# Kernel tuning notes

Hardware: AMD Instinct MI355X
Metric: run time of the kernel (lower is better)

The kernel has to match this reference:

```python
import jax, jax.numpy as jnp
import numpy as np

T, B, F, H, P = 256, 512, 256, 512, 12  # seq len, batch, feature_dim, hidden_dim, p_interval


def setup_inputs() -> dict:
    key = jax.random.key(0)
    ks = jax.random.split(key, 9)
    s = 1.0 / np.sqrt(F + H)  # torch Linear default init scale
    def lin(k):
        kw, kb = jax.random.split(k)
        W = jax.random.uniform(kw, (F + H, H), jnp.float32, -s, s)
        b = jax.random.uniform(kb, (H,), jnp.float32, -s, s)
        return W, b
    Wf, bf = lin(ks[0])
    Wi, bi = lin(ks[1])
    Wo, bo = lin(ks[2])
    Wg, bg = lin(ks[3])
    x = jax.random.normal(ks[4], (T, B, F), jnp.float32)
    return {"x": x, "Wf": Wf, "bf": bf, "Wi": Wi, "bi": bi,
            "Wo": Wo, "bo": bo, "Wg": Wg, "bg": bg}


def _slstm(x, Wf, bf, Wi, bi, Wo, bo, Wg, bg):
    Tn, Bn, _ = x.shape
    h0 = jnp.zeros((P, Bn, H), x.dtype)
    # NOTE: original torch code reassigns c to a 2D [B,H] tensor after step 0,
    # so c[t % P] indexes a batch ROW (shape [H]) that broadcasts. At t=0 the
    # slice is all-zeros either way, so carrying a 2D c is exactly faithful.
    c0 = jnp.zeros((Bn, H), x.dtype)

    def step(carry, inp):
        h, c = carry
        x_t, t = inp
        idx = t % P
        xc = jnp.concatenate([x_t, h[idx]], axis=1)  # [B, F+H]
        f = jax.nn.softmax(xc @ Wf + bf, axis=1)
        i = jax.nn.softmax(xc @ Wi + bi, axis=1)
        o = jax.nn.softmax(xc @ Wo + bo, axis=1)
        g = jnp.tanh(xc @ Wg + bg)
        c_new = jnp.tanh(f * c[idx] + i * g)  # c[idx]: row [H], broadcasts over B
        h = h.at[idx].set(o * c_new)
        return (h, c_new), None

    (h, _), _ = jax.lax.scan(step, (h0, c0), (x, jnp.arange(Tn)))
    return h[(Tn - 1) % P]


def reference(x, Wf, bf, Wi, bi, Wo, bo, Wg, bg):
    return _slstm(x, Wf, bf, Wi, bi, Wo, bo, Wg, bg)
```

## Files before the change

### kernel.cpp

```cpp
#include <hip/hip_runtime.h>

typedef unsigned short u16;
typedef unsigned int   u32;

typedef __attribute__((ext_vector_type(8))) short bf16x8;
typedef __attribute__((ext_vector_type(16))) float f32x16;

__device__ __forceinline__ u16 f2bf(float v) {
    u32 u = __float_as_uint(v);
    u32 r = (u + 0x7fffu + ((u >> 16) & 1u)) >> 16;
    return (u16)r;
}
__device__ __forceinline__ float bf2f(u16 h) { return __uint_as_float(((u32)h) << 16); }

__device__ __forceinline__ float ftanh(float x) {
    float e = __expf(2.0f * x);
    return 1.0f - 2.0f * __builtin_amdgcn_rcpf(e + 1.0f);
}

__device__ __forceinline__ void gl2lds16(const void* g, void* l) {
    __builtin_amdgcn_global_load_lds(
        (const __attribute__((address_space(1))) void*)g,
        (__attribute__((address_space(3))) void*)l, 16, 0, 0);
}

__global__ void init_k(u16* __restrict__ hh, u16* __restrict__ hl, float* __restrict__ cb) {
    int i = blockIdx.x * 256 + threadIdx.x;
    hh[i] = 0; hl[i] = 0;
    if (i < 2 * 512) cb[i] = 0.0f;
}

__global__ void pack_w(const float* __restrict__ Wf, const float* __restrict__ bf_,
                       const float* __restrict__ Wi, const float* __restrict__ bi_,
                       const float* __restrict__ Wo, const float* __restrict__ bo_,
                       const float* __restrict__ Wg, const float* __restrict__ bg_,
                       u16* __restrict__ wth, u16* __restrict__ wtl, float* __restrict__ bias4) {
    int idx = blockIdx.x * 256 + threadIdx.x;
    int n = idx / 768, k = idx - n * 768;
    int gate = n >> 9, col = n & 511;
    const float* W = (gate == 0) ? Wf : (gate == 1) ? Wi : (gate == 2) ? Wo : Wg;
    float v = W[k * 512 + col];
    u16 h = f2bf(v);
    wth[idx] = h;
    wtl[idx] = f2bf(v - bf2f(h));
    if (k == 0) {
        const float* bb = (gate == 0) ? bf_ : (gate == 1) ? bi_ : (gate == 2) ? bo_ : bg_;
        bias4[n] = bb[col];
    }
}

__global__ void split_x(const float* __restrict__ src, u16* __restrict__ oh, u16* __restrict__ ol) {
    int i = blockIdx.x * 256 + threadIdx.x;
    float4 v = ((const float4*)src)[i];
    u16 hx = f2bf(v.x), hy = f2bf(v.y), hz = f2bf(v.z), hw = f2bf(v.w);
    u16 lx = f2bf(v.x - bf2f(hx)), ly = f2bf(v.y - bf2f(hy));
    u16 lz = f2bf(v.z - bf2f(hz)), lw = f2bf(v.w - bf2f(hw));
    uint2 hv; hv.x = (u32)hx | ((u32)hy << 16); hv.y = (u32)hz | ((u32)hw << 16);
    uint2 lv; lv.x = (u32)lx | ((u32)ly << 16); lv.y = (u32)lz | ((u32)lw << 16);
    ((uint2*)oh)[i] = hv;
    ((uint2*)ol)[i] = lv;
}

#define BK 32
__global__ __launch_bounds__(256, 3) void gemm_x3(
    const u16* __restrict__ xh, const u16* __restrict__ xl,
    const u16* __restrict__ hh, const u16* __restrict__ hl,
    const u16* __restrict__ wth, const u16* __restrict__ wtl,
    const float* __restrict__ bias4, float* __restrict__ lg) {
    __shared__ __align__(16) u16 Ah[128 * BK];
    __shared__ __align__(16) u16 Al[128 * BK];
    __shared__ __align__(16) u16 Bh[128 * BK];
    __shared__ __align__(16) u16 Bl[128 * BK];

    const int tid = threadIdx.x;
    const int wid = tid >> 6, lane = tid & 63;
    const int bm = blockIdx.x, bn = blockIdx.y;
    const int s = bm >> 2;
    const int b0 = (bm & 3) * 128;
    const int laneR = lane >> 2;
    const int laneC = (lane & 3) * 8;

    u16* lds = (wid == 0) ? Ah : (wid == 1) ? Al : (wid == 2) ? Bh : Bl;
    const u16* xp = (wid == 0) ? xh : xl;
    const u16* hp = (wid == 0) ? hh : hl;
    const u16* wp = (wid == 2) ? wth : wtl;
    const u16* xrow = xp + (size_t)(s * 512 + b0) * 256 + laneR * 256 + laneC;
    const u16* hrow = hp + (size_t)(s * 512 + b0) * 512 + laneR * 512 + laneC;
    const u16* wrow = wp + (size_t)(bn * 128) * 768 + laneR * 768 + laneC;

    const int wm = wid >> 1, wn = wid & 1;
    const int l32 = lane & 31, khalf = lane >> 5;

    f32x16 acc[2][2];
#pragma unroll
    for (int i = 0; i < 2; i++)
#pragma unroll
        for (int j = 0; j < 2; j++)
#pragma unroll
            for (int r = 0; r < 16; ++r) acc[i][j][r] = 0.f;

    for (int k0 = 0; k0 < 768; k0 += BK) {
        __syncthreads();
        if (wid < 2) {
            if (k0 < 256) {
                const u16* src = xrow + k0;
#pragma unroll
                for (int r = 0; r < 8; ++r) gl2lds16(src + r * 16 * 256, lds + r * 16 * BK);
            } else {
                const u16* src = hrow + (k0 - 256);
#pragma unroll
                for (int r = 0; r < 8; ++r) gl2lds16(src + r * 16 * 512, lds + r * 16 * BK);
            }
        } else {
            const u16* src = wrow + k0;
#pragma unroll
            for (int r = 0; r < 8; ++r) gl2lds16(src + r * 16 * 768, lds + r * 16 * BK);
        }
        __syncthreads();

        bf16x8 a_h[2][2], a_l[2][2], b_h[2][2], b_l[2][2];
#pragma unroll
        for (int t = 0; t < 2; ++t)
#pragma unroll
            for (int ks = 0; ks < 2; ++ks) {
                int ko = ks * 16 + khalf * 8;
                a_h[t][ks] = *(const bf16x8*)&Ah[(wm * 64 + t * 32 + l32) * BK + ko];
                a_l[t][ks] = *(const bf16x8*)&Al[(wm * 64 + t * 32 + l32) * BK + ko];
                b_h[t][ks] = *(const bf16x8*)&Bh[(wn * 64 + t * 32 + l32) * BK + ko];
                b_l[t][ks] = *(const bf16x8*)&Bl[(wn * 64 + t * 32 + l32) * BK + ko];
            }
#pragma unroll
        for (int ks = 0; ks < 2; ++ks)
#pragma unroll
            for (int i = 0; i < 2; ++i)
#pragma unroll
                for (int j = 0; j < 2; ++j) {
                    acc[i][j] = __builtin_amdgcn_mfma_f32_32x32x16_bf16(a_h[i][ks], b_h[j][ks], acc[i][j], 0, 0, 0);
                    acc[i][j] = __builtin_amdgcn_mfma_f32_32x32x16_bf16(a_h[i][ks], b_l[j][ks], acc[i][j], 0, 0, 0);
                    acc[i][j] = __builtin_amdgcn_mfma_f32_32x32x16_bf16(a_l[i][ks], b_h[j][ks], acc[i][j], 0, 0, 0);
                }
    }

#pragma unroll
    for (int j = 0; j < 2; ++j) {
        int n = bn * 128 + wn * 64 + j * 32 + l32;
        float bv = bias4[n];
#pragma unroll
        for (int i = 0; i < 2; ++i) {
            int rbase = wm * 64 + i * 32 + 4 * khalf;
#pragma unroll
            for (int r = 0; r < 16; ++r) {
                int row = rbase + (r & 3) + 8 * (r >> 2);
                __builtin_nontemporal_store(acc[i][j][r] + bv,
                    &lg[(size_t)(bm * 128 + row) * 2048 + n]);
            }
        }
    }
}

__device__ __forceinline__ void chain_step(const float* __restrict__ lg, int j, int lane, float r[8]) {
    int rowb = (j + 1) % 12;
    const float* base = lg + (size_t)(j * 512 + rowb) * 2048 + lane * 8;
    float f[8], iv[8], g[8];
#pragma unroll
    for (int u = 0; u < 8; ++u) { f[u] = base[u]; iv[u] = base[512 + u]; g[u] = base[1536 + u]; }
    float mf = -1e30f, mi = -1e30f;
#pragma unroll
    for (int u = 0; u < 8; ++u) { mf = fmaxf(mf, f[u]); mi = fmaxf(mi, iv[u]); }
#pragma unroll
    for (int o = 32; o; o >>= 1) { mf = fmaxf(mf, __shfl_xor(mf, o)); mi = fmaxf(mi, __shfl_xor(mi, o)); }
    float sf = 0.f, si = 0.f;
#pragma unroll
    for (int u = 0; u < 8; ++u) {
        f[u] = __expf(f[u] - mf); sf += f[u];
        iv[u] = __expf(iv[u] - mi); si += iv[u];
    }
#pragma unroll
    for (int o = 32; o; o >>= 1) { sf += __shfl_xor(sf, o); si += __shfl_xor(si, o); }
    float rf = __builtin_amdgcn_rcpf(sf), ri = __builtin_amdgcn_rcpf(si);
#pragma unroll
    for (int u = 0; u < 8; ++u) {
        float gg = ftanh(g[u]);
        r[u] = ftanh(f[u] * rf * r[u] + iv[u] * ri * gg);
    }
}

__global__ __launch_bounds__(256) void gates_k(
    const float* __restrict__ lg, float* __restrict__ cb,
    u16* __restrict__ hh, u16* __restrict__ hl,
    float* __restrict__ out, int t0, int S, int rd, int wr) {
    __shared__ float rsh[512];
    const int widx = threadIdx.x >> 6, lane = threadIdx.x & 63;
    const int s = (S - 1) - (blockIdx.x >> 7);
    const int b = (blockIdx.x & 127) * 4 + widx;
    const int t = t0 + s;

    if (widx == 0) {
        float r[8];
#pragma unroll
        for (int u = 0; u < 8; ++u) r[u] = cb[rd * 512 + lane * 8 + u];
        for (int j = 0; j < s; ++j) chain_step(lg, j, lane, r);
#pragma unroll
        for (int u = 0; u < 8; ++u) rsh[lane * 8 + u] = r[u];
        if ((int)blockIdx.x == 127 && t0 + S < 256) {
            chain_step(lg, S - 1, lane, r);
#pragma unroll
            for (int u = 0; u < 8; ++u) cb[wr * 512 + lane * 8 + u] = r[u];
        }
    }
    __syncthreads();

    const float* row = lg + (size_t)(s * 512 + b) * 2048 + lane * 8;
    float f[8], iv[8], ov[8], g[8];
#pragma unroll
    for (int u = 0; u < 8; ++u) {
        f[u] = row[u]; iv[u] = row[512 + u]; ov[u] = row[1024 + u]; g[u] = row[1536 + u];
    }
    float mf = -1e30f, mi = -1e30f, mo = -1e30f;
#pragma unroll
    for (int u = 0; u < 8; ++u) { mf = fmaxf(mf, f[u]); mi = fmaxf(mi, iv[u]); mo = fmaxf(mo, ov[u]); }
#pragma unroll
    for (int o = 32; o; o >>= 1) {
        mf = fmaxf(mf, __shfl_xor(mf, o));
        mi = fmaxf(mi, __shfl_xor(mi, o));
        mo = fmaxf(mo, __shfl_xor(mo, o));
    }
    float sf = 0.f, si = 0.f, so = 0.f;
#pragma unroll
    for (int u = 0; u < 8; ++u) {
        f[u] = __expf(f[u] - mf); sf += f[u];
        iv[u] = __expf(iv[u] - mi); si += iv[u];
        ov[u] = __expf(ov[u] - mo); so += ov[u];
    }
#pragma unroll
    for (int o = 32; o; o >>= 1) {
        sf += __shfl_xor(sf, o); si += __shfl_xor(si, o); so += __shfl_xor(so, o);
    }
    float rf = __builtin_amdgcn_rcpf(sf), ri = __builtin_amdgcn_rcpf(si), ro = __builtin_amdgcn_rcpf(so);
    float hout[8];
#pragma unroll
    for (int u = 0; u < 8; ++u) {
        float rr = rsh[lane * 8 + u];
        float gg = ftanh(g[u]);
        float cv = ftanh(f[u] * rf * rr + iv[u] * ri * gg);
        hout[u] = ov[u] * ro * cv;
    }
    u32 hhp[4], hlp[4];
#pragma unroll
    for (int u = 0; u < 4; ++u) {
        u16 h0 = f2bf(hout[2 * u]), h1 = f2bf(hout[2 * u + 1]);
        u16 l0 = f2bf(hout[2 * u] - bf2f(h0)), l1 = f2bf(hout[2 * u + 1] - bf2f(h1));
        hhp[u] = (u32)h0 | ((u32)h1 << 16);
        hlp[u] = (u32)l0 | ((u32)l1 << 16);
    }
    size_t hb = ((size_t)(s * 512 + b)) * 512 + lane * 8;
    *(uint4*)&hh[hb] = make_uint4(hhp[0], hhp[1], hhp[2], hhp[3]);
    *(uint4*)&hl[hb] = make_uint4(hlp[0], hlp[1], hlp[2], hlp[3]);
    if (t == 255) {
        float* op = out + (size_t)b * 512 + lane * 8;
#pragma unroll
        for (int u = 0; u < 8; ++u) op[u] = hout[u];
    }
}

extern "C" void kernel_launch(void* const* d_in, const int* in_sizes, int n_in,
                              void* d_out, int out_size, void* d_ws, size_t ws_size,
                              hipStream_t stream) {
    const float* x   = (const float*)d_in[0];
    const float* Wf  = (const float*)d_in[1];
    const float* bf_ = (const float*)d_in[2];
    const float* Wi  = (const float*)d_in[3];
    const float* bi_ = (const float*)d_in[4];
    const float* Wo  = (const float*)d_in[5];
    const float* bo_ = (const float*)d_in[6];
    const float* Wg  = (const float*)d_in[7];
    const float* bg_ = (const float*)d_in[8];
    float* out = (float*)d_out;

    char* p = (char*)d_ws;
    u16* xh  = (u16*)p; p += 134217728;
    u16* xl  = (u16*)p; p += 134217728;
    u16* wth = (u16*)p; p += 3145728;
    u16* wtl = (u16*)p; p += 3145728;
    u16* hh  = (u16*)p; p += 6291456;
    u16* hl  = (u16*)p; p += 6291456;
    float* bias4 = (float*)p; p += 8192;
    float* cb    = (float*)p; p += 4096;
    float* lg    = (float*)p; p += 50331648;

    init_k<<<12288, 256, 0, stream>>>(hh, hl, cb);
    pack_w<<<6144, 256, 0, stream>>>(Wf, bf_, Wi, bi_, Wo, bo_, Wg, bg_, wth, wtl, bias4);
    split_x<<<32768, 256, 0, stream>>>(x, xh, xl);

    for (int blk = 0; blk < 22; ++blk) {
        int t0 = blk * 12;
        int S = (256 - t0 >= 12) ? 12 : (256 - t0);
        gemm_x3<<<dim3(S * 4, 16), 256, 0, stream>>>(
            xh + (size_t)t0 * 512 * 256, xl + (size_t)t0 * 512 * 256,
            hh, hl, wth, wtl, bias4, lg);
        gates_k<<<S * 128, 256, 0, stream>>>(lg, cb, hh, hl, out, t0, S, blk & 1, (blk + 1) & 1);
    }
}
```

Baseline: 2.029 ms.

## Rewrite split-bf16 GEMM with double-buffered LDS, larger tiles and grid swizzle

Replaces the 128x128 single-buffered GEMM with a 512-thread kernel using 192x256 tiles and double-buffered LDS. Global-to-LDS loads for the next k-tile are issued in two halves interleaved with the MFMA phases, using explicit vmcnt waits and barriers plus raised priority around the MFMA blocks. A 1D grid remapped across 8 column groups aims to improve L2 reuse. The M dimension is now bounds-checked because 192 does not divide evenly into it. The intent is to hide memory latency and raise MFMA utilisation, at the cost of more LDS and register pressure and more fragile hand-written synchronisation.

```diff
diff --git a/kernel.cpp b/kernel.cpp
--- a/kernel.cpp
+++ b/kernel.cpp
@@ -61,98 +61,170 @@
     ((uint2*)ol)[i] = lv;
 }
 
-#define BK 32
-__global__ __launch_bounds__(256, 3) void gemm_x3(
+#define KTILES 24
+#define BUFHALF 28672
+
+__global__ __launch_bounds__(512, 2) void gemm_p(
     const u16* __restrict__ xh, const u16* __restrict__ xl,
     const u16* __restrict__ hh, const u16* __restrict__ hl,
     const u16* __restrict__ wth, const u16* __restrict__ wtl,
-    const float* __restrict__ bias4, float* __restrict__ lg) {
-    __shared__ __align__(16) u16 Ah[128 * BK];
-    __shared__ __align__(16) u16 Al[128 * BK];
-    __shared__ __align__(16) u16 Bh[128 * BK];
-    __shared__ __align__(16) u16 Bl[128 * BK];
+    const float* __restrict__ bias4, float* __restrict__ lg,
+    int Mvalid, int gx) {
+    __shared__ __align__(16) u16 smem[2 * BUFHALF];
 
     const int tid = threadIdx.x;
     const int wid = tid >> 6, lane = tid & 63;
-    const int bm = blockIdx.x, bn = blockIdx.y;
-    const int s = bm >> 2;
-    const int b0 = (bm & 3) * 128;
-    const int laneR = lane >> 2;
-    const int laneC = (lane & 3) * 8;
-
-    u16* lds = (wid == 0) ? Ah : (wid == 1) ? Al : (wid == 2) ? Bh : Bl;
-    const u16* xp = (wid == 0) ? xh : xl;
-    const u16* hp = (wid == 0) ? hh : hl;
-    const u16* wp = (wid == 2) ? wth : wtl;
-    const u16* xrow = xp + (size_t)(s * 512 + b0) * 256 + laneR * 256 + laneC;
-    const u16* hrow = hp + (size_t)(s * 512 + b0) * 512 + laneR * 512 + laneC;
-    const u16* wrow = wp + (size_t)(bn * 128) * 768 + laneR * 768 + laneC;
-
-    const int wm = wid >> 1, wn = wid & 1;
     const int l32 = lane & 31, khalf = lane >> 5;
-
-    f32x16 acc[2][2];
-#pragma unroll
-    for (int i = 0; i < 2; i++)
-#pragma unroll
-        for (int j = 0; j < 2; j++)
+    const int wm = wid >> 2, wn = wid & 3;
+
+    const int wg = (blockIdx.x & 7) * gx + (blockIdx.x >> 3);
+    const int bm = wg % gx, bn = wg / gx;
+
+    const int laneK = (lane >> 4) * 8;
+    const int lr = lane & 15;
+    const u16* sp0[7]; const u16* sp1[7]; u32 slds[7]; bool sA[7];
+#pragma unroll
+    for (int j = 0; j < 7; ++j) {
+        int slot = wid * 7 + j;
+        int o, c;
+        if (slot < 12)      { o = 0; c = slot; }
+        else if (slot < 24) { o = 1; c = slot - 12; }
+        else if (slot < 40) { o = 2; c = slot - 24; }
+        else                { o = 3; c = slot - 40; }
+        if (o < 2) {
+            int row = bm * 192 + c * 16 + lr;
+            if (row >= Mvalid) row = Mvalid - 1;
+            sp0[j] = ((o == 0) ? xh : xl) + (size_t)row * 256 + laneK;
+            sp1[j] = ((o == 0) ? hh : hl) + (size_t)row * 512 + laneK;
+            sA[j] = true;
+            slds[j] = (o ? 6144u : 0u) + (u32)c * 512u;
+        } else {
+            int row = bn * 256 + c * 16 + lr;
+            sp0[j] = ((o == 2) ? wth : wtl) + (size_t)row * 768 + laneK;
+            sp1[j] = sp0[j];
+            sA[j] = false;
+            slds[j] = ((o == 2) ? 12288u : 20480u) + (u32)c * 512u;
+        }
+    }
+
+    u32 offA[3], offB[2];
+#pragma unroll
+    for (int i = 0; i < 3; ++i) {
+        int r = wm * 96 + i * 32 + l32;
+        offA[i] = (u32)((r >> 4) * 512 + (r & 15) * 8);
+    }
+#pragma unroll
+    for (int j = 0; j < 2; ++j) {
+        int r = wn * 64 + j * 32 + l32;
+        offB[j] = (u32)((r >> 4) * 512 + (r & 15) * 8);
+    }
+
+    f32x16 acc[3][2];
+#pragma unroll
+    for (int i = 0; i < 3; ++i)
+#pragma unroll
+        for (int j = 0; j < 2; ++j)
 #pragma unroll
             for (int r = 0; r < 16; ++r) acc[i][j][r] = 0.f;
 
-    for (int k0 = 0; k0 < 768; k0 += BK) {
-        __syncthreads();
-        if (wid < 2) {
-            if (k0 < 256) {
-                const u16* src = xrow + k0;
-#pragma unroll
-                for (int r = 0; r < 8; ++r) gl2lds16(src + r * 16 * 256, lds + r * 16 * BK);
-            } else {
-                const u16* src = hrow + (k0 - 256);
-#pragma unroll
-                for (int r = 0; r < 8; ++r) gl2lds16(src + r * 16 * 512, lds + r * 16 * BK);
-            }
+#pragma unroll
+    for (int j = 0; j < 7; ++j) gl2lds16(sp0[j], smem + slds[j]);
+
+#pragma unroll 2
+    for (int kk = 0; kk < KTILES; ++kk) {
+        u16* bufc = smem + (kk & 1) * BUFHALF;
+        u16* bufo = smem + ((kk & 1) ^ 1) * BUFHALF;
+        const int kn = (kk + 1) * 32;
+
+        if (kk < KTILES - 1) {
+#pragma unroll
+            for (int j = 0; j < 4; ++j) {
+                const u16* src = sA[j] ? ((kn < 256) ? sp0[j] + kn : sp1[j] + (kn - 256))
+                                       : (sp0[j] + kn);
+                gl2lds16(src, bufo + slds[j]);
+            }
+            asm volatile("s_waitcnt vmcnt(4)" ::: "memory");
         } else {
-            const u16* src = wrow + k0;
-#pragma unroll
-            for (int r = 0; r < 8; ++r) gl2lds16(src + r * 16 * 768, lds + r * 16 * BK);
-        }
-        __syncthreads();
-
-        bf16x8 a_h[2][2], a_l[2][2], b_h[2][2], b_l[2][2];
-#pragma unroll
-        for (int t = 0; t < 2; ++t)
-#pragma unroll
-            for (int ks = 0; ks < 2; ++ks) {
-                int ko = ks * 16 + khalf * 8;
-                a_h[t][ks] = *(const bf16x8*)&Ah[(wm * 64 + t * 32 + l32) * BK + ko];
-                a_l[t][ks] = *(const bf16x8*)&Al[(wm * 64 + t * 32 + l32) * BK + ko];
-                b_h[t][ks] = *(const bf16x8*)&Bh[(wn * 64 + t * 32 + l32) * BK + ko];
-                b_l[t][ks] = *(const bf16x8*)&Bl[(wn * 64 + t * 32 + l32) * BK + ko];
-            }
-#pragma unroll
-        for (int ks = 0; ks < 2; ++ks)
-#pragma unroll
-            for (int i = 0; i < 2; ++i)
-#pragma unroll
-                for (int j = 0; j < 2; ++j) {
-                    acc[i][j] = __builtin_amdgcn_mfma_f32_32x32x16_bf16(a_h[i][ks], b_h[j][ks], acc[i][j], 0, 0, 0);
-                    acc[i][j] = __builtin_amdgcn_mfma_f32_32x32x16_bf16(a_h[i][ks], b_l[j][ks], acc[i][j], 0, 0, 0);
-                    acc[i][j] = __builtin_amdgcn_mfma_f32_32x32x16_bf16(a_l[i][ks], b_h[j][ks], acc[i][j], 0, 0, 0);
-                }
+            asm volatile("s_waitcnt vmcnt(0)" ::: "memory");
+        }
+        asm volatile("s_barrier" ::: "memory");
+
+        bf16x8 ah[3], al[3], bh[2], bl[2];
+        {
+            const u32 q = (u32)(khalf) * 128u;
+#pragma unroll
+            for (int i = 0; i < 3; ++i) {
+                ah[i] = *(const bf16x8*)(bufc + offA[i] + q);
+                al[i] = *(const bf16x8*)(bufc + 6144 + offA[i] + q);
+            }
+#pragma unroll
+            for (int j = 0; j < 2; ++j) {
+                bh[j] = *(const bf16x8*)(bufc + 12288 + offB[j] + q);
+                bl[j] = *(const bf16x8*)(bufc + 20480 + offB[j] + q);
+            }
+        }
+        asm volatile("s_waitcnt lgkmcnt(0)" ::: "memory");
+        __builtin_amdgcn_s_setprio(1);
+#pragma unroll
+        for (int i = 0; i < 3; ++i)
+#pragma unroll
+            for (int j = 0; j < 2; ++j) {
+                acc[i][j] = __builtin_amdgcn_mfma_f32_32x32x16_bf16(ah[i], bh[j], acc[i][j], 0, 0, 0);
+                acc[i][j] = __builtin_amdgcn_mfma_f32_32x32x16_bf16(ah[i], bl[j], acc[i][j], 0, 0, 0);
+                acc[i][j] = __builtin_amdgcn_mfma_f32_32x32x16_bf16(al[i], bh[j], acc[i][j], 0, 0, 0);
+            }
+        __builtin_amdgcn_s_setprio(0);
+        asm volatile("s_barrier" ::: "memory");
+
+        if (kk < KTILES - 1) {
+#pragma unroll
+            for (int j = 4; j < 7; ++j) {
+                const u16* src = sA[j] ? ((kn < 256) ? sp0[j] + kn : sp1[j] + (kn - 256))
+                                       : (sp0[j] + kn);
+                gl2lds16(src, bufo + slds[j]);
+            }
+        }
+        {
+            const u32 q = (u32)(2 + khalf) * 128u;
+#pragma unroll
+            for (int i = 0; i < 3; ++i) {
+                ah[i] = *(const bf16x8*)(bufc + offA[i] + q);
+                al[i] = *(const bf16x8*)(bufc + 6144 + offA[i] + q);
+            }
+#pragma unroll
+            for (int j = 0; j < 2; ++j) {
+                bh[j] = *(const bf16x8*)(bufc + 12288 + offB[j] + q);
+                bl[j] = *(const bf16x8*)(bufc + 20480 + offB[j] + q);
+            }
+        }
+        asm volatile("s_barrier" ::: "memory");
+        asm volatile("s_waitcnt lgkmcnt(0)" ::: "memory");
+        __builtin_amdgcn_s_setprio(1);
+#pragma unroll
+        for (int i = 0; i < 3; ++i)
+#pragma unroll
+            for (int j = 0; j < 2; ++j) {
+                acc[i][j] = __builtin_amdgcn_mfma_f32_32x32x16_bf16(ah[i], bh[j], acc[i][j], 0, 0, 0);
+                acc[i][j] = __builtin_amdgcn_mfma_f32_32x32x16_bf16(ah[i], bl[j], acc[i][j], 0, 0, 0);
+                acc[i][j] = __builtin_amdgcn_mfma_f32_32x32x16_bf16(al[i], bh[j], acc[i][j], 0, 0, 0);
+            }
+        __builtin_amdgcn_s_setprio(0);
+        asm volatile("s_barrier" ::: "memory");
     }
 
 #pragma unroll
     for (int j = 0; j < 2; ++j) {
-        int n = bn * 128 + wn * 64 + j * 32 + l32;
+        int n = bn * 256 + wn * 64 + j * 32 + l32;
         float bv = bias4[n];
 #pragma unroll
-        for (int i = 0; i < 2; ++i) {
-            int rbase = wm * 64 + i * 32 + 4 * khalf;
+        for (int i = 0; i < 3; ++i) {
+            int rbase = bm * 192 + wm * 96 + i * 32 + 4 * khalf;
 #pragma unroll
             for (int r = 0; r < 16; ++r) {
                 int row = rbase + (r & 3) + 8 * (r >> 2);
-                __builtin_nontemporal_store(acc[i][j][r] + bv,
-                    &lg[(size_t)(bm * 128 + row) * 2048 + n]);
+                if (row < Mvalid)
+                    __builtin_nontemporal_store(acc[i][j][r] + bv,
+                        &lg[(size_t)row * 2048 + n]);
             }
         }
     }
@@ -295,9 +367,11 @@
     for (int blk = 0; blk < 22; ++blk) {
         int t0 = blk * 12;
         int S = (256 - t0 >= 12) ? 12 : (256 - t0);
-        gemm_x3<<<dim3(S * 4, 16), 256, 0, stream>>>(
+        int M = S * 512;
+        int gx = (M + 191) / 192;
+        gemm_p<<<gx * 8, 512, 0, stream>>>(
             xh + (size_t)t0 * 512 * 256, xl + (size_t)t0 * 512 * 256,
-            hh, hl, wth, wtl, bias4, lg);
+            hh, hl, wth, wtl, bias4, lg, M, gx);
         gates_k<<<S * 128, 256, 0, stream>>>(lg, cb, hh, hl, out, t0, S, blk & 1, (blk + 1) & 1);
     }
 }
```

Result: slower. 2.104 ms (+3.7%).

## Rewrite split-bf16 GEMM with larger tiles, triple-buffered swizzled LDS, and pre-concatenated K

Applied to the files above, without the earlier changes.

Replaces the 128x128 tile GEMM with a 192x256 tile using 8 waves and 512 threads. The three-product split-bf16 scheme is reformulated as one long K=2304 GEMM: the weights are packed with hi/lo/hi copies so the A side can stream xh/xl/hh/hl segments. A and B tiles are loaded into LDS asynchronously with an XOR swizzle, A is triple-buffered and B double-buffered, and loads are overlapped with MFMA using waitcnt and setprio. Blocks are remapped onto XCDs and edge rows are masked. The cost is three times the weight storage and more complex, hand-scheduled synchronization.

```diff
diff --git a/kernel.cpp b/kernel.cpp
--- a/kernel.cpp
+++ b/kernel.cpp
@@ -30,19 +30,25 @@
     if (i < 2 * 512) cb[i] = 0.0f;
 }
 
-__global__ void pack_w(const float* __restrict__ Wf, const float* __restrict__ bf_,
-                       const float* __restrict__ Wi, const float* __restrict__ bi_,
-                       const float* __restrict__ Wo, const float* __restrict__ bo_,
-                       const float* __restrict__ Wg, const float* __restrict__ bg_,
-                       u16* __restrict__ wth, u16* __restrict__ wtl, float* __restrict__ bias4) {
+__global__ void pack_wq(const float* __restrict__ Wf, const float* __restrict__ bf_,
+                        const float* __restrict__ Wi, const float* __restrict__ bi_,
+                        const float* __restrict__ Wo, const float* __restrict__ bo_,
+                        const float* __restrict__ Wg, const float* __restrict__ bg_,
+                        u16* __restrict__ wq, float* __restrict__ bias4) {
     int idx = blockIdx.x * 256 + threadIdx.x;
     int n = idx / 768, k = idx - n * 768;
     int gate = n >> 9, col = n & 511;
     const float* W = (gate == 0) ? Wf : (gate == 1) ? Wi : (gate == 2) ? Wo : Wg;
     float v = W[k * 512 + col];
     u16 h = f2bf(v);
-    wth[idx] = h;
-    wtl[idx] = f2bf(v - bf2f(h));
+    u16 l = f2bf(v - bf2f(h));
+    size_t base = (size_t)n * 2304;
+    if (k < 256) {
+        wq[base + k] = h; wq[base + 512 + k] = h; wq[base + 256 + k] = l;
+    } else {
+        int d = k - 256;
+        wq[base + 768 + d] = h; wq[base + 1792 + d] = h; wq[base + 1280 + d] = l;
+    }
     if (k == 0) {
         const float* bb = (gate == 0) ? bf_ : (gate == 1) ? bi_ : (gate == 2) ? bo_ : bg_;
         bias4[n] = bb[col];
@@ -61,98 +67,161 @@
     ((uint2*)ol)[i] = lv;
 }
 
-#define BK 32
-__global__ __launch_bounds__(256, 3) void gemm_x3(
+#define KT 36
+__global__ __launch_bounds__(512, 2) void gemm_q(
     const u16* __restrict__ xh, const u16* __restrict__ xl,
     const u16* __restrict__ hh, const u16* __restrict__ hl,
-    const u16* __restrict__ wth, const u16* __restrict__ wtl,
-    const float* __restrict__ bias4, float* __restrict__ lg) {
-    __shared__ __align__(16) u16 Ah[128 * BK];
-    __shared__ __align__(16) u16 Al[128 * BK];
-    __shared__ __align__(16) u16 Bh[128 * BK];
-    __shared__ __align__(16) u16 Bl[128 * BK];
+    const u16* __restrict__ wq, const float* __restrict__ bias4,
+    float* __restrict__ lg, int Mvalid, int gx) {
+    __shared__ __align__(16) u16 smem[69632];
 
     const int tid = threadIdx.x;
     const int wid = tid >> 6, lane = tid & 63;
-    const int bm = blockIdx.x, bn = blockIdx.y;
-    const int s = bm >> 2;
-    const int b0 = (bm & 3) * 128;
-    const int laneR = lane >> 2;
-    const int laneC = (lane & 3) * 8;
-
-    u16* lds = (wid == 0) ? Ah : (wid == 1) ? Al : (wid == 2) ? Bh : Bl;
-    const u16* xp = (wid == 0) ? xh : xl;
-    const u16* hp = (wid == 0) ? hh : hl;
-    const u16* wp = (wid == 2) ? wth : wtl;
-    const u16* xrow = xp + (size_t)(s * 512 + b0) * 256 + laneR * 256 + laneC;
-    const u16* hrow = hp + (size_t)(s * 512 + b0) * 512 + laneR * 512 + laneC;
-    const u16* wrow = wp + (size_t)(bn * 128) * 768 + laneR * 768 + laneC;
-
-    const int wm = wid >> 1, wn = wid & 1;
     const int l32 = lane & 31, khalf = lane >> 5;
-
-    f32x16 acc[2][2];
-#pragma unroll
-    for (int i = 0; i < 2; i++)
-#pragma unroll
-        for (int j = 0; j < 2; j++)
+    const int wm = wid >> 2, wn = wid & 3;
+
+    int bm, bn;
+    if (gx == 32) { int xcd = blockIdx.x & 7, r = blockIdx.x >> 3; bm = xcd * 4 + (r & 3); bn = r >> 2; }
+    else          { bm = blockIdx.x % gx; bn = blockIdx.x / gx; }
+
+    const int lr8 = lane >> 3;
+    const int ksw = ((lane & 7) ^ (lr8 & 7)) * 8;
+
+    int arowc[3]; size_t brow[4];
+#pragma unroll
+    for (int c = 0; c < 3; ++c) {
+        int row = bm * 192 + (wid * 3 + c) * 8 + lr8;
+        if (row >= Mvalid) row = Mvalid - 1;
+        arowc[c] = row;
+    }
+#pragma unroll
+    for (int c = 0; c < 4; ++c)
+        brow[c] = (size_t)(bn * 256 + (wid * 4 + c) * 8 + lr8) * 2304;
+
+#define STAGE_A(kt, dstoff) do {                                              \
+        int kt_ = (kt); const u16* base_; int str_, ko_;                      \
+        if (kt_ < 12) { base_ = (kt_ >= 8) ? xl : xh; str_ = 256; ko_ = (kt_ & 3) * 64; } \
+        else { int sub_ = kt_ - 12; base_ = (sub_ >= 16) ? hl : hh; str_ = 512; ko_ = (sub_ & 7) * 64; } \
+        _Pragma("unroll")                                                     \
+        for (int c_ = 0; c_ < 3; ++c_)                                        \
+            gl2lds16(base_ + (size_t)arowc[c_] * str_ + ko_ + ksw,            \
+                     smem + (dstoff) + (wid * 3 + c_) * 512 + lane * 8);      \
+    } while (0)
+
+#define STAGE_B(kt, dstoff) do {                                              \
+        _Pragma("unroll")                                                     \
+        for (int c_ = 0; c_ < 4; ++c_)                                        \
+            gl2lds16(wq + brow[c_] + (kt) * 64 + ksw,                         \
+                     smem + (dstoff) + (wid * 4 + c_) * 512 + lane * 8);      \
+    } while (0)
+
+    u32 offA[3][4], offB[2][4];
+#pragma unroll
+    for (int i = 0; i < 3; ++i) {
+        int row = wm * 96 + i * 32 + l32;
+        u32 rsw = (u32)(row & 7) << 3;
+#pragma unroll
+        for (int ks = 0; ks < 4; ++ks)
+            offA[i][ks] = (u32)row * 64 + (((u32)(ks * 16 + khalf * 8)) ^ rsw);
+    }
+#pragma unroll
+    for (int j = 0; j < 2; ++j) {
+        int row = wn * 64 + j * 32 + l32;
+        u32 rsw = (u32)(row & 7) << 3;
+#pragma unroll
+        for (int ks = 0; ks < 4; ++ks)
+            offB[j][ks] = (u32)row * 64 + (((u32)(ks * 16 + khalf * 8)) ^ rsw);
+    }
+
+    f32x16 acc[3][2];
+#pragma unroll
+    for (int i = 0; i < 3; ++i)
+#pragma unroll
+        for (int j = 0; j < 2; ++j)
 #pragma unroll
             for (int r = 0; r < 16; ++r) acc[i][j][r] = 0.f;
 
-    for (int k0 = 0; k0 < 768; k0 += BK) {
-        __syncthreads();
-        if (wid < 2) {
-            if (k0 < 256) {
-                const u16* src = xrow + k0;
-#pragma unroll
-                for (int r = 0; r < 8; ++r) gl2lds16(src + r * 16 * 256, lds + r * 16 * BK);
-            } else {
-                const u16* src = hrow + (k0 - 256);
-#pragma unroll
-                for (int r = 0; r < 8; ++r) gl2lds16(src + r * 16 * 512, lds + r * 16 * BK);
-            }
+    STAGE_A(0, 0);
+    STAGE_B(0, 36864);
+    STAGE_A(1, 12288);
+
+    int aoff = 0;
+    for (int kt = 0; kt < KT; ++kt) {
+        const int boff = 36864 + ((kt & 1) << 14);
+        if (kt + 1 < KT) {
+            STAGE_B(kt + 1, 36864 + (((kt + 1) & 1) << 14));
+            asm volatile("s_waitcnt vmcnt(7)" ::: "memory");
         } else {
-            const u16* src = wrow + k0;
-#pragma unroll
-            for (int r = 0; r < 8; ++r) gl2lds16(src + r * 16 * 768, lds + r * 16 * BK);
+            asm volatile("s_waitcnt vmcnt(0)" ::: "memory");
         }
-        __syncthreads();
-
-        bf16x8 a_h[2][2], a_l[2][2], b_h[2][2], b_l[2][2];
-#pragma unroll
-        for (int t = 0; t < 2; ++t)
-#pragma unroll
-            for (int ks = 0; ks < 2; ++ks) {
-                int ko = ks * 16 + khalf * 8;
-                a_h[t][ks] = *(const bf16x8*)&Ah[(wm * 64 + t * 32 + l32) * BK + ko];
-                a_l[t][ks] = *(const bf16x8*)&Al[(wm * 64 + t * 32 + l32) * BK + ko];
-                b_h[t][ks] = *(const bf16x8*)&Bh[(wn * 64 + t * 32 + l32) * BK + ko];
-                b_l[t][ks] = *(const bf16x8*)&Bl[(wn * 64 + t * 32 + l32) * BK + ko];
-            }
+        __builtin_amdgcn_s_barrier();
+        __builtin_amdgcn_sched_barrier(0);
+
+        const u16* At = smem + aoff;
+        const u16* Bt = smem + boff;
+
+        bf16x8 a0[3][2], b0[2][2];
+#pragma unroll
+        for (int i = 0; i < 3; ++i)
+#pragma unroll
+            for (int ks = 0; ks < 2; ++ks) a0[i][ks] = *(const bf16x8*)(At + offA[i][ks]);
+#pragma unroll
+        for (int j = 0; j < 2; ++j)
+#pragma unroll
+            for (int ks = 0; ks < 2; ++ks) b0[j][ks] = *(const bf16x8*)(Bt + offB[j][ks]);
+        __builtin_amdgcn_s_setprio(1);
 #pragma unroll
         for (int ks = 0; ks < 2; ++ks)
 #pragma unroll
-            for (int i = 0; i < 2; ++i)
-#pragma unroll
-                for (int j = 0; j < 2; ++j) {
-                    acc[i][j] = __builtin_amdgcn_mfma_f32_32x32x16_bf16(a_h[i][ks], b_h[j][ks], acc[i][j], 0, 0, 0);
-                    acc[i][j] = __builtin_amdgcn_mfma_f32_32x32x16_bf16(a_h[i][ks], b_l[j][ks], acc[i][j], 0, 0, 0);
-                    acc[i][j] = __builtin_amdgcn_mfma_f32_32x32x16_bf16(a_l[i][ks], b_h[j][ks], acc[i][j], 0, 0, 0);
-                }
-    }
+            for (int i = 0; i < 3; ++i)
+#pragma unroll
+                for (int j = 0; j < 2; ++j)
+                    acc[i][j] = __builtin_amdgcn_mfma_f32_32x32x16_bf16(a0[i][ks], b0[j][ks], acc[i][j], 0, 0, 0);
+        __builtin_amdgcn_s_setprio(0);
+
+        if (kt + 2 < KT) {
+            int adst = aoff + 24576; if (adst >= 36864) adst -= 36864;
+            STAGE_A(kt + 2, adst);
+        }
+
+        bf16x8 a1[3][2], b1[2][2];
+#pragma unroll
+        for (int i = 0; i < 3; ++i)
+#pragma unroll
+            for (int ks = 0; ks < 2; ++ks) a1[i][ks] = *(const bf16x8*)(At + offA[i][ks + 2]);
+#pragma unroll
+        for (int j = 0; j < 2; ++j)
+#pragma unroll
+            for (int ks = 0; ks < 2; ++ks) b1[j][ks] = *(const bf16x8*)(Bt + offB[j][ks + 2]);
+        __builtin_amdgcn_s_setprio(1);
+#pragma unroll
+        for (int ks = 0; ks < 2; ++ks)
+#pragma unroll
+            for (int i = 0; i < 3; ++i)
+#pragma unroll
+                for (int j = 0; j < 2; ++j)
+                    acc[i][j] = __builtin_amdgcn_mfma_f32_32x32x16_bf16(a1[i][ks], b1[j][ks], acc[i][j], 0, 0, 0);
+        __builtin_amdgcn_s_setprio(0);
+
+        __builtin_amdgcn_s_barrier();
+        __builtin_amdgcn_sched_barrier(0);
+        aoff += 12288; if (aoff == 36864) aoff = 0;
+    }
+#undef STAGE_A
+#undef STAGE_B
 
 #pragma unroll
     for (int j = 0; j < 2; ++j) {
-        int n = bn * 128 + wn * 64 + j * 32 + l32;
+        int n = bn * 256 + wn * 64 + j * 32 + l32;
         float bv = bias4[n];
 #pragma unroll
-        for (int i = 0; i < 2; ++i) {
-            int rbase = wm * 64 + i * 32 + 4 * khalf;
+        for (int i = 0; i < 3; ++i) {
+            int rbase = bm * 192 + wm * 96 + i * 32 + 4 * khalf;
 #pragma unroll
             for (int r = 0; r < 16; ++r) {
                 int row = rbase + (r & 3) + 8 * (r >> 2);
-                __builtin_nontemporal_store(acc[i][j][r] + bv,
-                    &lg[(size_t)(bm * 128 + row) * 2048 + n]);
+                if (row < Mvalid)
+                    lg[(size_t)row * 2048 + n] = acc[i][j][r] + bv;
             }
         }
     }
@@ -280,8 +349,7 @@
     char* p = (char*)d_ws;
     u16* xh  = (u16*)p; p += 134217728;
     u16* xl  = (u16*)p; p += 134217728;
-    u16* wth = (u16*)p; p += 3145728;
-    u16* wtl = (u16*)p; p += 3145728;
+    u16* wq  = (u16*)p; p += 9437184;
     u16* hh  = (u16*)p; p += 6291456;
     u16* hl  = (u16*)p; p += 6291456;
     float* bias4 = (float*)p; p += 8192;
@@ -289,15 +357,17 @@
     float* lg    = (float*)p; p += 50331648;
 
     init_k<<<12288, 256, 0, stream>>>(hh, hl, cb);
-    pack_w<<<6144, 256, 0, stream>>>(Wf, bf_, Wi, bi_, Wo, bo_, Wg, bg_, wth, wtl, bias4);
+    pack_wq<<<6144, 256, 0, stream>>>(Wf, bf_, Wi, bi_, Wo, bo_, Wg, bg_, wq, bias4);
     split_x<<<32768, 256, 0, stream>>>(x, xh, xl);
 
     for (int blk = 0; blk < 22; ++blk) {
         int t0 = blk * 12;
         int S = (256 - t0 >= 12) ? 12 : (256 - t0);
-        gemm_x3<<<dim3(S * 4, 16), 256, 0, stream>>>(
+        int M = S * 512;
+        int gx = (M + 191) / 192;
+        gemm_q<<<gx * 8, 512, 0, stream>>>(
             xh + (size_t)t0 * 512 * 256, xl + (size_t)t0 * 512 * 256,
-            hh, hl, wth, wtl, bias4, lg);
+            hh, hl, wq, bias4, lg, M, gx);
         gates_k<<<S * 128, 256, 0, stream>>>(lg, cb, hh, hl, out, t0, S, blk & 1, (blk + 1) & 1);
     }
 }
```

Result: no change. 2.053 ms (+1.2%).

## Rewrite split-bf16 GEMM as 256x256 double-buffered K-concatenated tile kernel

Applied to the files above, without the earlier changes.

Replaces the 128x128 three-product bf16x3 GEMM with a 256x256 tile, 512-thread kernel. The three hi/lo products are folded into one longer K dimension by pre-packing the weights as [h, l, h] segments, so each MFMA pass is a plain bf16 GEMM over K=2304. The kernel adds double-buffered LDS staging with XOR swizzle, interleaved staged loads and 16x16x32 MFMAs with barriers and priority hints, and an XCD-aware block mapping. The aim is better data reuse and latency hiding. The cost is triple-sized packed weights, higher register and LDS pressure (128KB LDS), and fewer blocks per launch for the small M dimension.

```diff
diff --git a/kernel.cpp b/kernel.cpp
--- a/kernel.cpp
+++ b/kernel.cpp
@@ -4,7 +4,7 @@
 typedef unsigned int   u32;
 
 typedef __attribute__((ext_vector_type(8))) short bf16x8;
-typedef __attribute__((ext_vector_type(16))) float f32x16;
+typedef __attribute__((ext_vector_type(4))) float f32x4;
 
 __device__ __forceinline__ u16 f2bf(float v) {
     u32 u = __float_as_uint(v);
@@ -30,19 +30,25 @@
     if (i < 2 * 512) cb[i] = 0.0f;
 }
 
-__global__ void pack_w(const float* __restrict__ Wf, const float* __restrict__ bf_,
-                       const float* __restrict__ Wi, const float* __restrict__ bi_,
-                       const float* __restrict__ Wo, const float* __restrict__ bo_,
-                       const float* __restrict__ Wg, const float* __restrict__ bg_,
-                       u16* __restrict__ wth, u16* __restrict__ wtl, float* __restrict__ bias4) {
+__global__ void pack_wq(const float* __restrict__ Wf, const float* __restrict__ bf_,
+                        const float* __restrict__ Wi, const float* __restrict__ bi_,
+                        const float* __restrict__ Wo, const float* __restrict__ bo_,
+                        const float* __restrict__ Wg, const float* __restrict__ bg_,
+                        u16* __restrict__ wq, float* __restrict__ bias4) {
     int idx = blockIdx.x * 256 + threadIdx.x;
     int n = idx / 768, k = idx - n * 768;
     int gate = n >> 9, col = n & 511;
     const float* W = (gate == 0) ? Wf : (gate == 1) ? Wi : (gate == 2) ? Wo : Wg;
     float v = W[k * 512 + col];
     u16 h = f2bf(v);
-    wth[idx] = h;
-    wtl[idx] = f2bf(v - bf2f(h));
+    u16 l = f2bf(v - bf2f(h));
+    size_t base = (size_t)n * 2304;
+    if (k < 256) {
+        wq[base + k] = h; wq[base + 512 + k] = h; wq[base + 256 + k] = l;
+    } else {
+        int d = k - 256;
+        wq[base + 768 + d] = h; wq[base + 1792 + d] = h; wq[base + 1280 + d] = l;
+    }
     if (k == 0) {
         const float* bb = (gate == 0) ? bf_ : (gate == 1) ? bi_ : (gate == 2) ? bo_ : bg_;
         bias4[n] = bb[col];
@@ -61,99 +67,151 @@
     ((uint2*)ol)[i] = lv;
 }
 
-#define BK 32
-__global__ __launch_bounds__(256, 3) void gemm_x3(
+#define KT 36
+__global__ __launch_bounds__(512, 2) void gemm_q(
     const u16* __restrict__ xh, const u16* __restrict__ xl,
     const u16* __restrict__ hh, const u16* __restrict__ hl,
-    const u16* __restrict__ wth, const u16* __restrict__ wtl,
-    const float* __restrict__ bias4, float* __restrict__ lg) {
-    __shared__ __align__(16) u16 Ah[128 * BK];
-    __shared__ __align__(16) u16 Al[128 * BK];
-    __shared__ __align__(16) u16 Bh[128 * BK];
-    __shared__ __align__(16) u16 Bl[128 * BK];
+    const u16* __restrict__ wq, const float* __restrict__ bias4,
+    float* __restrict__ lg, int gx) {
+    __shared__ __align__(16) u16 smem[65536];
 
     const int tid = threadIdx.x;
     const int wid = tid >> 6, lane = tid & 63;
-    const int bm = blockIdx.x, bn = blockIdx.y;
-    const int s = bm >> 2;
-    const int b0 = (bm & 3) * 128;
-    const int laneR = lane >> 2;
-    const int laneC = (lane & 3) * 8;
-
-    u16* lds = (wid == 0) ? Ah : (wid == 1) ? Al : (wid == 2) ? Bh : Bl;
-    const u16* xp = (wid == 0) ? xh : xl;
-    const u16* hp = (wid == 0) ? hh : hl;
-    const u16* wp = (wid == 2) ? wth : wtl;
-    const u16* xrow = xp + (size_t)(s * 512 + b0) * 256 + laneR * 256 + laneC;
-    const u16* hrow = hp + (size_t)(s * 512 + b0) * 512 + laneR * 512 + laneC;
-    const u16* wrow = wp + (size_t)(bn * 128) * 768 + laneR * 768 + laneC;
-
-    const int wm = wid >> 1, wn = wid & 1;
-    const int l32 = lane & 31, khalf = lane >> 5;
-
-    f32x16 acc[2][2];
-#pragma unroll
-    for (int i = 0; i < 2; i++)
-#pragma unroll
-        for (int j = 0; j < 2; j++)
-#pragma unroll
-            for (int r = 0; r < 16; ++r) acc[i][j][r] = 0.f;
-
-    for (int k0 = 0; k0 < 768; k0 += BK) {
-        __syncthreads();
-        if (wid < 2) {
-            if (k0 < 256) {
-                const u16* src = xrow + k0;
-#pragma unroll
-                for (int r = 0; r < 8; ++r) gl2lds16(src + r * 16 * 256, lds + r * 16 * BK);
-            } else {
-                const u16* src = hrow + (k0 - 256);
-#pragma unroll
-                for (int r = 0; r < 8; ++r) gl2lds16(src + r * 16 * 512, lds + r * 16 * BK);
-            }
-        } else {
-            const u16* src = wrow + k0;
-#pragma unroll
-            for (int r = 0; r < 8; ++r) gl2lds16(src + r * 16 * 768, lds + r * 16 * BK);
+    const int l15 = lane & 15, l4 = lane >> 4;
+    const int wm = wid >> 2, wn = wid & 3;
+
+    const int xcd = blockIdx.x & 7, rr_ = blockIdx.x >> 3;
+    const int bmp = gx >> 3;
+    const int bm = xcd * bmp + (rr_ % bmp);
+    const int bn = rr_ / bmp;
+
+    u32 aox[2][2], aoh[2][2], adst[2][2];
+    u32 boff[2][2], bdst[2][2];
+#pragma unroll
+    for (int q = 0; q < 2; ++q) {
+        u32 idx = (u32)q * 512 + (u32)tid;
+        u32 ro = idx >> 3, s = idx & 7, c = s ^ (ro & 7);
+#pragma unroll
+        for (int u = 0; u < 2; ++u) {
+            u32 arow = (u32)bm * 256 + (ro & 63) + (ro >> 6) * 128 + (u32)u * 64;
+            u32 alds = ((ro & 63) + (ro >> 6) * 128 + (u32)u * 64) * 64 + s * 8;
+            aox[u][q] = arow * 256 + c * 8;
+            aoh[u][q] = arow * 512 + c * 8;
+            adst[u][q] = alds;
+            u32 bcol = (u32)bn * 256 + (u32)u * 128 + ro;
+            boff[u][q] = bcol * 2304 + c * 8;
+            bdst[u][q] = 16384 + ((u32)u * 128 + ro) * 64 + s * 8;
         }
-        __syncthreads();
-
-        bf16x8 a_h[2][2], a_l[2][2], b_h[2][2], b_l[2][2];
-#pragma unroll
-        for (int t = 0; t < 2; ++t)
-#pragma unroll
-            for (int ks = 0; ks < 2; ++ks) {
-                int ko = ks * 16 + khalf * 8;
-                a_h[t][ks] = *(const bf16x8*)&Ah[(wm * 64 + t * 32 + l32) * BK + ko];
-                a_l[t][ks] = *(const bf16x8*)&Al[(wm * 64 + t * 32 + l32) * BK + ko];
-                b_h[t][ks] = *(const bf16x8*)&Bh[(wn * 64 + t * 32 + l32) * BK + ko];
-                b_l[t][ks] = *(const bf16x8*)&Bl[(wn * 64 + t * 32 + l32) * BK + ko];
-            }
-#pragma unroll
-        for (int ks = 0; ks < 2; ++ks)
-#pragma unroll
-            for (int i = 0; i < 2; ++i)
-#pragma unroll
-                for (int j = 0; j < 2; ++j) {
-                    acc[i][j] = __builtin_amdgcn_mfma_f32_32x32x16_bf16(a_h[i][ks], b_h[j][ks], acc[i][j], 0, 0, 0);
-                    acc[i][j] = __builtin_amdgcn_mfma_f32_32x32x16_bf16(a_h[i][ks], b_l[j][ks], acc[i][j], 0, 0, 0);
-                    acc[i][j] = __builtin_amdgcn_mfma_f32_32x32x16_bf16(a_l[i][ks], b_h[j][ks], acc[i][j], 0, 0, 0);
-                }
-    }
-
-#pragma unroll
-    for (int j = 0; j < 2; ++j) {
-        int n = bn * 128 + wn * 64 + j * 32 + l32;
+    }
+
+    u32 rA[8], rB[4], sK[2];
+#pragma unroll
+    for (int f = 0; f < 8; ++f) rA[f] = (u32)(wm * 128 + f * 16 + l15) * 64;
+#pragma unroll
+    for (int f = 0; f < 4; ++f) rB[f] = 16384u + (u32)(wn * 64 + f * 16 + l15) * 64;
+#pragma unroll
+    for (int ks = 0; ks < 2; ++ks) sK[ks] = (u32)(((ks * 4 + l4) ^ (lane & 7)) * 8);
+
+    f32x4 acc[8][4];
+#pragma unroll
+    for (int f = 0; f < 8; ++f)
+#pragma unroll
+        for (int j = 0; j < 4; ++j) { acc[f][j].x = 0.f; acc[f][j].y = 0.f; acc[f][j].z = 0.f; acc[f][j].w = 0.f; }
+
+    bf16x8 aH[4], bF[4];
+
+#define STAGE_B(u) do {                                                       \
+        gl2lds16(bsr + boff[u][0], smem + nb32 + bdst[u][0]);                 \
+        gl2lds16(bsr + boff[u][1], smem + nb32 + bdst[u][1]); } while (0)
+#define STAGE_A(u) do {                                                       \
+        gl2lds16(as_ + (xp ? aox[u][0] : aoh[u][0]) + ako, smem + nb32 + adst[u][0]); \
+        gl2lds16(as_ + (xp ? aox[u][1] : aoh[u][1]) + ako, smem + nb32 + adst[u][1]); } while (0)
+#define RD_A(h, ks) do {                                                      \
+        aH[0] = *(const bf16x8*)(smem + cb32 + rA[(h)*4+0] + sK[ks]);         \
+        aH[1] = *(const bf16x8*)(smem + cb32 + rA[(h)*4+1] + sK[ks]);         \
+        aH[2] = *(const bf16x8*)(smem + cb32 + rA[(h)*4+2] + sK[ks]);         \
+        aH[3] = *(const bf16x8*)(smem + cb32 + rA[(h)*4+3] + sK[ks]); } while (0)
+#define RD_B(ks) do {                                                         \
+        bF[0] = *(const bf16x8*)(smem + cb32 + rB[0] + sK[ks]);               \
+        bF[1] = *(const bf16x8*)(smem + cb32 + rB[1] + sK[ks]);               \
+        bF[2] = *(const bf16x8*)(smem + cb32 + rB[2] + sK[ks]);               \
+        bF[3] = *(const bf16x8*)(smem + cb32 + rB[3] + sK[ks]); } while (0)
+#define MM16(hb) do {                                                         \
+        __builtin_amdgcn_s_setprio(1);                                        \
+        _Pragma("unroll")                                                     \
+        for (int fi_ = 0; fi_ < 4; ++fi_)                                     \
+            _Pragma("unroll")                                                 \
+            for (int fj_ = 0; fj_ < 4; ++fj_)                                 \
+                acc[(hb)*4+fi_][fj_] = __builtin_amdgcn_mfma_f32_16x16x32_bf16(\
+                    aH[fi_], bF[fj_], acc[(hb)*4+fi_][fj_], 0, 0, 0);         \
+        __builtin_amdgcn_s_setprio(0);                                        \
+    } while (0)
+#define BAR() do { __builtin_amdgcn_s_barrier(); __builtin_amdgcn_sched_barrier(0); } while (0)
+
+    {
+        const int nb32 = 0;
+        const u16* bsr = wq;
+        const u16* as_ = xh; const u32 ako = 0; const bool xp = true;
+        STAGE_B(0); STAGE_B(1); STAGE_A(0); STAGE_A(1);
+    }
+    asm volatile("s_waitcnt vmcnt(2)" ::: "memory");
+    BAR();
+
+#pragma unroll 2
+    for (int kt = 0; kt < KT; ++kt) {
+        const int cb32 = (kt & 1) << 15;
+        const int nb32 = cb32 ^ 32768;
+        const int kn = kt + 1;
+        const bool stg = (kn < KT);
+        const u16* as_ = xh; u32 ako = 0; bool xp = true;
+        if (stg) {
+            if (kn < 12) { as_ = (kn >= 8) ? xl : xh; ako = (u32)(kn & 3) * 64; xp = true; }
+            else { int s2 = kn - 12; as_ = (s2 >= 16) ? hl : hh; ako = (u32)(s2 & 7) * 64; xp = false; }
+        }
+        const u16* bsr = wq + (size_t)kn * 64;
+
+        if (stg) STAGE_B(0);
+        RD_B(0); RD_A(0, 0);
+        BAR();
+        MM16(0);
+        if (stg) asm volatile("s_waitcnt vmcnt(2)" ::: "memory");
+        else     asm volatile("s_waitcnt vmcnt(0)" ::: "memory");
+        BAR();
+        if (stg) STAGE_B(1);
+        RD_A(1, 0);
+        BAR();
+        MM16(1);
+        BAR();
+        if (stg) STAGE_A(0);
+        RD_B(1); RD_A(0, 1);
+        BAR();
+        MM16(0);
+        BAR();
+        if (stg) STAGE_A(1);
+        RD_A(1, 1);
+        BAR();
+        MM16(1);
+        if (stg) asm volatile("s_waitcnt vmcnt(2)" ::: "memory");
+        BAR();
+    }
+#undef STAGE_B
+#undef STAGE_A
+#undef RD_A
+#undef RD_B
+#undef MM16
+#undef BAR
+
+#pragma unroll
+    for (int fj = 0; fj < 4; ++fj) {
+        int n = bn * 256 + wn * 64 + fj * 16 + l15;
         float bv = bias4[n];
 #pragma unroll
-        for (int i = 0; i < 2; ++i) {
-            int rbase = wm * 64 + i * 32 + 4 * khalf;
-#pragma unroll
-            for (int r = 0; r < 16; ++r) {
-                int row = rbase + (r & 3) + 8 * (r >> 2);
-                __builtin_nontemporal_store(acc[i][j][r] + bv,
-                    &lg[(size_t)(bm * 128 + row) * 2048 + n]);
-            }
+        for (int f = 0; f < 8; ++f) {
+            int row = bm * 256 + wm * 128 + f * 16 + l4 * 4;
+            lg[(size_t)(row + 0) * 2048 + n] = acc[f][fj].x + bv;
+            lg[(size_t)(row + 1) * 2048 + n] = acc[f][fj].y + bv;
+            lg[(size_t)(row + 2) * 2048 + n] = acc[f][fj].z + bv;
+            lg[(size_t)(row + 3) * 2048 + n] = acc[f][fj].w + bv;
         }
     }
 }
@@ -280,8 +338,7 @@
     char* p = (char*)d_ws;
     u16* xh  = (u16*)p; p += 134217728;
     u16* xl  = (u16*)p; p += 134217728;
-    u16* wth = (u16*)p; p += 3145728;
-    u16* wtl = (u16*)p; p += 3145728;
+    u16* wq  = (u16*)p; p += 9437184;
     u16* hh  = (u16*)p; p += 6291456;
     u16* hl  = (u16*)p; p += 6291456;
     float* bias4 = (float*)p; p += 8192;
@@ -289,15 +346,17 @@
     float* lg    = (float*)p; p += 50331648;
 
     init_k<<<12288, 256, 0, stream>>>(hh, hl, cb);
-    pack_w<<<6144, 256, 0, stream>>>(Wf, bf_, Wi, bi_, Wo, bo_, Wg, bg_, wth, wtl, bias4);
+    pack_wq<<<6144, 256, 0, stream>>>(Wf, bf_, Wi, bi_, Wo, bo_, Wg, bg_, wq, bias4);
     split_x<<<32768, 256, 0, stream>>>(x, xh, xl);
 
     for (int blk = 0; blk < 22; ++blk) {
         int t0 = blk * 12;
         int S = (256 - t0 >= 12) ? 12 : (256 - t0);
-        gemm_x3<<<dim3(S * 4, 16), 256, 0, stream>>>(
+        int M = S * 512;
+        int gx = M / 256;
+        gemm_q<<<gx * 8, 512, 0, stream>>>(
             xh + (size_t)t0 * 512 * 256, xl + (size_t)t0 * 512 * 256,
-            hh, hl, wth, wtl, bias4, lg);
+            hh, hl, wq, bias4, lg, gx);
         gates_k<<<S * 128, 256, 0, stream>>>(lg, cb, hh, hl, out, t0, S, blk & 1, (blk + 1) & 1);
     }
 }
```

New measurement: 2.007 ms. About the same (-1.1%).
